# Optimization experiments

Measured on AMD Instinct MI355X. Metric: run time of the kernel, lower is better.

## Reference

```python
import jax, jax.numpy as jnp
import numpy as np

B, F, P = 16384, 4096, 32
D = F // P
EPS = 1e-5


def setup_inputs() -> dict:
    key = jax.random.key(0)
    ks = jax.random.split(key, 5)
    bound = 1.0 / np.sqrt(D)
    return {
        "x": jax.random.normal(ks[0], (B, F), dtype=jnp.float32),
        "weights1": jax.random.uniform(ks[1], (P, D, D), dtype=jnp.float32, minval=-bound, maxval=bound),
        "bias1": jax.random.uniform(ks[2], (F,), dtype=jnp.float32, minval=-bound, maxval=bound),
        "weights2": jax.random.uniform(ks[3], (P, D, D), dtype=jnp.float32, minval=-bound, maxval=bound),
        "bias2": jax.random.uniform(ks[4], (F,), dtype=jnp.float32, minval=-bound, maxval=bound),
        "gamma1": jnp.ones((F,), dtype=jnp.float32),
        "beta1": jnp.zeros((F,), dtype=jnp.float32),
        "gamma3": jnp.ones((F,), dtype=jnp.float32),
        "beta3": jnp.zeros((F,), dtype=jnp.float32),
    }


def _block_matmul(x, w):
    # x: [B, F] viewed as [B, P, D]; w: [P, D, D] block-diagonal blocks.
    # Equivalent to x @ block_diag(*w) without building the [F, F] matrix.
    xb = x.reshape(x.shape[0], P, D)
    return jnp.einsum("bpd,pde->bpe", xb, w).reshape(x.shape[0], F)


def _batchnorm(y, gamma, beta):
    # Training-mode BatchNorm1d: biased variance over the batch dim.
    mean = jnp.mean(y, axis=0)
    var = jnp.var(y, axis=0)
    return gamma * (y - mean) * jax.lax.rsqrt(var + EPS) + beta


def reference(x, weights1, bias1, weights2, bias2, gamma1, beta1, gamma3, beta3):
    o1 = jnp.tanh(_batchnorm(_block_matmul(x, weights1) + bias1, gamma1, beta1))
    o2 = _block_matmul(o1, weights2) + bias2
    o3 = jnp.tanh(_batchnorm(o2 + x, gamma3, beta3))
    return o3
```

## Files before the change

### kernel.cpp

```cpp
#include <hip/hip_runtime.h>
#include <hip/hip_bf16.h>
#include <cstdint>
#include <cstddef>

#define B_ 16384
#define F_ 4096
#define P_ 32
#define D_ 128
#define STRIPS 32
#define ITERS 8

using f32x4 = __attribute__((ext_vector_type(4))) float;
using s16x8 = __attribute__((ext_vector_type(8))) short;

union abuf { s16x8 v; uint32_t u[4]; };

__device__ inline uint32_t pk_bf16(float a, float b) {
    float2 f; f.x = a; f.y = b;
    union { __hip_bfloat162 h; uint32_t u; } cv;
    cv.h = __float22bfloat162_rn(f);
    return cv.u;
}
__device__ inline float tanh_e(float ze) {
    float e = __builtin_amdgcn_exp2f(ze);
    return 1.f - 2.f * __builtin_amdgcn_rcpf(e + 1.f);
}

__device__ inline void stage_wp(const float* __restrict__ Wp, short* s_w, int tid) {
#pragma unroll
    for (int it = 0; it < 8; ++it) {
        int slot = it * 256 + tid;
        int l15 = slot & 15;
        int l4  = (slot >> 4) & 3;
        int sp  = (slot >> 6) & 3;
        int j   = slot >> 8;
        const float* s0 = Wp + (size_t)(sp * 32 + l4 * 4) * D_ + j * 16 + l15;
        const float* s1 = s0 + (size_t)16 * D_;
        abuf a;
        a.u[0] = pk_bf16(s0[0],            s0[(size_t)D_]);
        a.u[1] = pk_bf16(s0[(size_t)2*D_], s0[(size_t)3*D_]);
        a.u[2] = pk_bf16(s1[0],            s1[(size_t)D_]);
        a.u[3] = pk_bf16(s1[(size_t)2*D_], s1[(size_t)3*D_]);
        *(s16x8*)((char*)s_w + (size_t)slot * 16) = a.v;
    }
}

__global__ __launch_bounds__(256, 3) void k_stats1(
    const float* __restrict__ x, const float* __restrict__ W1,
    float* __restrict__ gsum, float* __restrict__ gsq)
{
    __shared__ short s_w[D_ * D_];
    __shared__ float s_sum[D_], s_sq[D_];
    const int tid = threadIdx.x;
    const int p = blockIdx.x / STRIPS, strip = blockIdx.x % STRIPS;
    stage_wp(W1 + (size_t)p * D_ * D_, s_w, tid);
    if (tid < D_) { s_sum[tid] = 0.f; s_sq[tid] = 0.f; }
    __syncthreads();
    const int wave = tid >> 6, lane = tid & 63;
    const int l15 = lane & 15, l4 = lane >> 4;
    const int ldsb = lane * 16;

    f32x4 csum[8], csq[8];
#pragma unroll
    for (int j = 0; j < 8; ++j) { csum[j] = (f32x4){0,0,0,0}; csq[j] = (f32x4){0,0,0,0}; }

    for (int it = 0; it < ITERS; ++it) {
        const int g = strip * 32 + it * 4 + wave;
        const float* ap = x + (size_t)(g * 16 + l15) * F_ + p * D_ + l4 * 4;
        f32x4 xv[8];
#pragma unroll
        for (int j = 0; j < 8; ++j)
            xv[j] = __builtin_nontemporal_load((const f32x4*)(ap + j * 16));
        abuf a[4];
#pragma unroll
        for (int s = 0; s < 4; ++s) {
            a[s].u[0] = pk_bf16(xv[2*s][0],   xv[2*s][1]);
            a[s].u[1] = pk_bf16(xv[2*s][2],   xv[2*s][3]);
            a[s].u[2] = pk_bf16(xv[2*s+1][0], xv[2*s+1][1]);
            a[s].u[3] = pk_bf16(xv[2*s+1][2], xv[2*s+1][3]);
        }
        f32x4 acc[8];
#pragma unroll
        for (int j = 0; j < 8; ++j) acc[j] = (f32x4){0,0,0,0};
#pragma unroll
        for (int s = 0; s < 4; ++s)
#pragma unroll
            for (int j = 0; j < 8; ++j) {
                s16x8 w = *(const s16x8*)((const char*)s_w + (j * 4 + s) * 1024 + ldsb);
                acc[j] = __builtin_amdgcn_mfma_f32_16x16x32_bf16(w, a[s].v, acc[j], 0, 0, 0);
            }
#pragma unroll
        for (int j = 0; j < 8; ++j)
#pragma unroll
            for (int r = 0; r < 4; ++r) {
                float v = acc[j][r];
                csum[j][r] += v;
                csq[j][r] = fmaf(v, v, csq[j][r]);
            }
    }
#pragma unroll
    for (int j = 0; j < 8; ++j)
#pragma unroll
        for (int r = 0; r < 4; ++r) {
            float sm = csum[j][r], q = csq[j][r];
            sm += __shfl_xor(sm, 1); q += __shfl_xor(q, 1);
            sm += __shfl_xor(sm, 2); q += __shfl_xor(q, 2);
            sm += __shfl_xor(sm, 4); q += __shfl_xor(q, 4);
            sm += __shfl_xor(sm, 8); q += __shfl_xor(q, 8);
            if (l15 == 0) {
                atomicAdd(&s_sum[j * 16 + l4 * 4 + r], sm);
                atomicAdd(&s_sq [j * 16 + l4 * 4 + r], q);
            }
        }
    __syncthreads();
    if (tid < D_) {
        atomicAdd(&gsum[p * D_ + tid], s_sum[tid]);
        atomicAdd(&gsq [p * D_ + tid], s_sq[tid]);
    }
}

__global__ __launch_bounds__(256, 2) void k_fused(
    const float* __restrict__ x, float* __restrict__ yf,
    const float* __restrict__ W1, const float* __restrict__ W2,
    const float* __restrict__ sce, const float* __restrict__ she,
    float* __restrict__ gsum, float* __restrict__ gsq)
{
    __shared__ short s_w1[D_ * D_];
    __shared__ short s_w2[D_ * D_];
    __shared__ float s_sc[D_], s_sh[D_];
    __shared__ float s_sum[D_], s_sq[D_];
    const int tid = threadIdx.x;
    const int p = blockIdx.x / STRIPS, strip = blockIdx.x % STRIPS;
    stage_wp(W1 + (size_t)p * D_ * D_, s_w1, tid);
    stage_wp(W2 + (size_t)p * D_ * D_, s_w2, tid);
    if (tid < D_) {
        s_sc[tid] = sce[p * D_ + tid];
        s_sh[tid] = she[p * D_ + tid];
        s_sum[tid] = 0.f; s_sq[tid] = 0.f;
    }
    __syncthreads();
    const int wave = tid >> 6, lane = tid & 63;
    const int l15 = lane & 15, l4 = lane >> 4;
    const int ldsb = lane * 16;

    f32x4 csum[8], csq[8];
#pragma unroll
    for (int j = 0; j < 8; ++j) { csum[j] = (f32x4){0,0,0,0}; csq[j] = (f32x4){0,0,0,0}; }

    auto LOADX = [&](f32x4 (&xv)[8], int it) {
        const int g = strip * 32 + it * 4 + wave;
        const float* ap = x + (size_t)(g * 16 + l15) * F_ + p * D_ + l4 * 4;
#pragma unroll
        for (int j = 0; j < 8; ++j)
            xv[j] = __builtin_nontemporal_load((const f32x4*)(ap + j * 16));
    };

    auto TILE = [&](f32x4 (&xv)[8], int it) {
        abuf a[4];
#pragma unroll
        for (int s = 0; s < 4; ++s) {
            a[s].u[0] = pk_bf16(xv[2*s][0],   xv[2*s][1]);
            a[s].u[1] = pk_bf16(xv[2*s][2],   xv[2*s][3]);
            a[s].u[2] = pk_bf16(xv[2*s+1][0], xv[2*s+1][1]);
            a[s].u[3] = pk_bf16(xv[2*s+1][2], xv[2*s+1][3]);
        }
        f32x4 acc[8];
#pragma unroll
        for (int j = 0; j < 8; ++j) acc[j] = (f32x4){0,0,0,0};
#pragma unroll
        for (int s = 0; s < 4; ++s)
#pragma unroll
            for (int j = 0; j < 8; ++j) {
                s16x8 w = *(const s16x8*)((const char*)s_w1 + (j * 4 + s) * 1024 + ldsb);
                acc[j] = __builtin_amdgcn_mfma_f32_16x16x32_bf16(w, a[s].v, acc[j], 0, 0, 0);
            }
#pragma unroll
        for (int sp = 0; sp < 4; ++sp) {
            const int kb = sp * 32 + l4 * 4;
            f32x4 sc0 = *(const f32x4*)&s_sc[kb], sc1 = *(const f32x4*)&s_sc[kb + 16];
            f32x4 sh0 = *(const f32x4*)&s_sh[kb], sh1 = *(const f32x4*)&s_sh[kb + 16];
            float t0[4], t1[4];
#pragma unroll
            for (int q = 0; q < 4; ++q) {
                t0[q] = tanh_e(fmaf(acc[2*sp][q],   sc0[q], sh0[q]));
                t1[q] = tanh_e(fmaf(acc[2*sp+1][q], sc1[q], sh1[q]));
            }
            a[sp].u[0] = pk_bf16(t0[0], t0[1]);
            a[sp].u[1] = pk_bf16(t0[2], t0[3]);
            a[sp].u[2] = pk_bf16(t1[0], t1[1]);
            a[sp].u[3] = pk_bf16(t1[2], t1[3]);
        }
#pragma unroll
        for (int j = 0; j < 8; ++j) acc[j] = (f32x4){0,0,0,0};
#pragma unroll
        for (int sp = 0; sp < 4; ++sp)
#pragma unroll
            for (int j = 0; j < 8; ++j) {
                s16x8 w = *(const s16x8*)((const char*)s_w2 + (j * 4 + sp) * 1024 + ldsb);
                acc[j] = __builtin_amdgcn_mfma_f32_16x16x32_bf16(w, a[sp].v, acc[j], 0, 0, 0);
            }
        const int g = strip * 32 + it * 4 + wave;
        float* rp = yf + (size_t)(g * 16 + l15) * F_ + p * D_ + l4 * 4;
#pragma unroll
        for (int j = 0; j < 8; ++j) {
            f32x4 o;
#pragma unroll
            for (int r = 0; r < 4; ++r) {
                float v = acc[j][r] + xv[j][r];
                o[r] = v;
                csum[j][r] += v;
                csq[j][r] = fmaf(v, v, csq[j][r]);
            }
            __builtin_nontemporal_store(o, (f32x4*)(rp + j * 16));
        }
    };

    f32x4 xv0[8], xv1[8];
    LOADX(xv0, 0);
#pragma unroll
    for (int h = 0; h < 4; ++h) {
        LOADX(xv1, 2 * h + 1);
        TILE(xv0, 2 * h);
        if (h < 3) LOADX(xv0, 2 * h + 2);
        TILE(xv1, 2 * h + 1);
    }

#pragma unroll
    for (int j = 0; j < 8; ++j)
#pragma unroll
        for (int r = 0; r < 4; ++r) {
            float sm = csum[j][r], q = csq[j][r];
            sm += __shfl_xor(sm, 1); q += __shfl_xor(q, 1);
            sm += __shfl_xor(sm, 2); q += __shfl_xor(q, 2);
            sm += __shfl_xor(sm, 4); q += __shfl_xor(q, 4);
            sm += __shfl_xor(sm, 8); q += __shfl_xor(q, 8);
            if (l15 == 0) {
                atomicAdd(&s_sum[j * 16 + l4 * 4 + r], sm);
                atomicAdd(&s_sq [j * 16 + l4 * 4 + r], q);
            }
        }
    __syncthreads();
    if (tid < D_) {
        atomicAdd(&gsum[p * D_ + tid], s_sum[tid]);
        atomicAdd(&gsq [p * D_ + tid], s_sq[tid]);
    }
}

__global__ void k_finalize(const float* __restrict__ sum,
                           const float* __restrict__ sumsq,
                           const float* __restrict__ gamma,
                           const float* __restrict__ beta,
                           float* __restrict__ sce, float* __restrict__ she)
{
    const float L2E2 = 2.f * 1.44269504088896340736f;
    int f = blockIdx.x * blockDim.x + threadIdx.x;
    if (f < F_) {
        float mean = sum[f] * (1.f / B_);
        float var  = sumsq[f] * (1.f / B_) - mean * mean;
        float rstd = rsqrtf(var + 1e-5f);
        float sc = gamma[f] * rstd;
        sce[f] = L2E2 * sc;
        she[f] = L2E2 * (beta[f] - mean * sc);
    }
}

__global__ void k_bn_tanh(float* yb, const float* __restrict__ sce,
                          const float* __restrict__ she)
{
    const size_t n4 = (size_t)B_ * F_ / 4;
    size_t i = (size_t)blockIdx.x * blockDim.x + threadIdx.x;
    const size_t stride = (size_t)gridDim.x * blockDim.x;
    for (; i < n4; i += stride) {
        f32x4 v = __builtin_nontemporal_load((const f32x4*)yb + i);
        int col = (int)((i * 4) & (F_ - 1));
        f32x4 sc = *(const f32x4*)(sce + col);
        f32x4 sh = *(const f32x4*)(she + col);
        f32x4 r;
#pragma unroll
        for (int t = 0; t < 4; ++t) r[t] = tanh_e(fmaf(v[t], sc[t], sh[t]));
        __builtin_nontemporal_store(r, (f32x4*)yb + i);
    }
}

extern "C" void kernel_launch(void* const* d_in, const int* in_sizes, int n_in,
                              void* d_out, int out_size, void* d_ws, size_t ws_size,
                              hipStream_t stream) {
    const float* x      = (const float*)d_in[0];
    const float* W1     = (const float*)d_in[1];
    const float* W2     = (const float*)d_in[3];
    const float* gamma1 = (const float*)d_in[5];
    const float* beta1  = (const float*)d_in[6];
    const float* gamma3 = (const float*)d_in[7];
    const float* beta3  = (const float*)d_in[8];

    float* yf = (float*)d_out;
    float* S  = (float*)d_ws;
    float* sum1 = S;
    float* sq1  = S + 4096;
    float* sum3 = S + 8192;
    float* sq3  = S + 12288;
    float* sce1 = S + 16384;
    float* she1 = S + 20480;
    float* sce3 = S + 24576;
    float* she3 = S + 28672;

    hipMemsetAsync(d_ws, 0, 4 * 4096 * sizeof(float), stream);

    k_stats1<<<P_ * STRIPS, 256, 0, stream>>>(x, W1, sum1, sq1);
    k_finalize<<<F_ / 256, 256, 0, stream>>>(sum1, sq1, gamma1, beta1, sce1, she1);
    k_fused<<<P_ * STRIPS, 256, 0, stream>>>(x, yf, W1, W2, sce1, she1, sum3, sq3);
    k_finalize<<<F_ / 256, 256, 0, stream>>>(sum3, sq3, gamma3, beta3, sce3, she3);
    k_bn_tanh<<<4096, 256, 0, stream>>>(yf, sce3, she3);
}
```

Measured before the change: 627.2 us.

## Store pre-BN intermediate as fp16 in workspace and software-pipeline stats1 loads

The fused kernel now writes the pre-normalization residual sum as fp16 into workspace rather than fp32 into the output, and the final BN+tanh pass reads fp16 and writes fp32 output. This halves the intermediate's write and read traffic, at the cost of fp16 rounding before normalization. The first stats kernel also gets double-buffered x loads with occupancy hint lowered to 2, and nontemporal hints are dropped on x loads. The fp16 path runs only if the workspace is large enough.

```diff
diff --git a/kernel.cpp b/kernel.cpp
--- a/kernel.cpp
+++ b/kernel.cpp
@@ -1,5 +1,6 @@
 #include <hip/hip_runtime.h>
 #include <hip/hip_bf16.h>
+#include <hip/hip_fp16.h>
 #include <cstdint>
 #include <cstddef>
 
@@ -20,6 +21,16 @@
     union { __hip_bfloat162 h; uint32_t u; } cv;
     cv.h = __float22bfloat162_rn(f);
     return cv.u;
+}
+__device__ inline uint32_t pk_f16(float a, float b) {
+    float2 f; f.x = a; f.y = b;
+    union { __half2 h; uint32_t u; } cv;
+    cv.h = __float22half2_rn(f);
+    return cv.u;
+}
+__device__ inline float f16_f32(unsigned short h) {
+    union { unsigned short u; __half h; } cv; cv.u = h;
+    return __half2float(cv.h);
 }
 __device__ inline float tanh_e(float ze) {
     float e = __builtin_amdgcn_exp2f(ze);
@@ -45,7 +56,7 @@
     }
 }
 
-__global__ __launch_bounds__(256, 3) void k_stats1(
+__global__ __launch_bounds__(256, 2) void k_stats1(
     const float* __restrict__ x, const float* __restrict__ W1,
     float* __restrict__ gsum, float* __restrict__ gsq)
 {
@@ -64,13 +75,15 @@
 #pragma unroll
     for (int j = 0; j < 8; ++j) { csum[j] = (f32x4){0,0,0,0}; csq[j] = (f32x4){0,0,0,0}; }
 
-    for (int it = 0; it < ITERS; ++it) {
+    auto LOADX = [&](f32x4 (&xv)[8], int it) {
         const int g = strip * 32 + it * 4 + wave;
         const float* ap = x + (size_t)(g * 16 + l15) * F_ + p * D_ + l4 * 4;
-        f32x4 xv[8];
 #pragma unroll
         for (int j = 0; j < 8; ++j)
-            xv[j] = __builtin_nontemporal_load((const f32x4*)(ap + j * 16));
+            xv[j] = *(const f32x4*)(ap + j * 16);
+    };
+
+    auto TILE = [&](f32x4 (&xv)[8]) {
         abuf a[4];
 #pragma unroll
         for (int s = 0; s < 4; ++s) {
@@ -97,7 +110,18 @@
                 csum[j][r] += v;
                 csq[j][r] = fmaf(v, v, csq[j][r]);
             }
-    }
+    };
+
+    f32x4 xv0[8], xv1[8];
+    LOADX(xv0, 0);
+#pragma unroll
+    for (int h = 0; h < 4; ++h) {
+        LOADX(xv1, 2 * h + 1);
+        TILE(xv0);
+        if (h < 3) LOADX(xv0, 2 * h + 2);
+        TILE(xv1);
+    }
+
 #pragma unroll
     for (int j = 0; j < 8; ++j)
 #pragma unroll
@@ -119,8 +143,10 @@
     }
 }
 
+template<bool FH>
 __global__ __launch_bounds__(256, 2) void k_fused(
     const float* __restrict__ x, float* __restrict__ yf,
+    unsigned short* __restrict__ yh,
     const float* __restrict__ W1, const float* __restrict__ W2,
     const float* __restrict__ sce, const float* __restrict__ she,
     float* __restrict__ gsum, float* __restrict__ gsq)
@@ -152,7 +178,7 @@
         const float* ap = x + (size_t)(g * 16 + l15) * F_ + p * D_ + l4 * 4;
 #pragma unroll
         for (int j = 0; j < 8; ++j)
-            xv[j] = __builtin_nontemporal_load((const f32x4*)(ap + j * 16));
+            xv[j] = *(const f32x4*)(ap + j * 16);
     };
 
     auto TILE = [&](f32x4 (&xv)[8], int it) {
@@ -200,7 +226,7 @@
                 acc[j] = __builtin_amdgcn_mfma_f32_16x16x32_bf16(w, a[sp].v, acc[j], 0, 0, 0);
             }
         const int g = strip * 32 + it * 4 + wave;
-        float* rp = yf + (size_t)(g * 16 + l15) * F_ + p * D_ + l4 * 4;
+        const size_t rowoff = (size_t)(g * 16 + l15) * F_ + p * D_ + l4 * 4;
 #pragma unroll
         for (int j = 0; j < 8; ++j) {
             f32x4 o;
@@ -211,7 +237,15 @@
                 csum[j][r] += v;
                 csq[j][r] = fmaf(v, v, csq[j][r]);
             }
-            __builtin_nontemporal_store(o, (f32x4*)(rp + j * 16));
+            if (FH) {
+                uint32_t h2[2];
+                h2[0] = pk_f16(o[0], o[1]);
+                h2[1] = pk_f16(o[2], o[3]);
+                __builtin_nontemporal_store(*(const uint64_t*)h2,
+                                            (uint64_t*)(yh + rowoff + j * 16));
+            } else {
+                __builtin_nontemporal_store(o, (f32x4*)(yf + rowoff + j * 16));
+            }
         }
     };
 
@@ -264,21 +298,44 @@
     }
 }
 
-__global__ void k_bn_tanh(float* yb, const float* __restrict__ sce,
+template<bool FH>
+__global__ void k_bn_tanh(const unsigned short* __restrict__ yh,
+                          float* __restrict__ out,
+                          const float* __restrict__ sce,
                           const float* __restrict__ she)
 {
-    const size_t n4 = (size_t)B_ * F_ / 4;
-    size_t i = (size_t)blockIdx.x * blockDim.x + threadIdx.x;
-    const size_t stride = (size_t)gridDim.x * blockDim.x;
-    for (; i < n4; i += stride) {
-        f32x4 v = __builtin_nontemporal_load((const f32x4*)yb + i);
-        int col = (int)((i * 4) & (F_ - 1));
-        f32x4 sc = *(const f32x4*)(sce + col);
-        f32x4 sh = *(const f32x4*)(she + col);
-        f32x4 r;
-#pragma unroll
-        for (int t = 0; t < 4; ++t) r[t] = tanh_e(fmaf(v[t], sc[t], sh[t]));
-        __builtin_nontemporal_store(r, (f32x4*)yb + i);
+    if (FH) {
+        const size_t n8 = (size_t)B_ * F_ / 8;
+        size_t i = (size_t)blockIdx.x * blockDim.x + threadIdx.x;
+        const size_t stride = (size_t)gridDim.x * blockDim.x;
+        for (; i < n8; i += stride) {
+            s16x8 hv = *(const s16x8*)(yh + i * 8);
+            int col = (int)((i * 8) & (F_ - 1));
+            f32x4 sc0 = *(const f32x4*)(sce + col), sc1 = *(const f32x4*)(sce + col + 4);
+            f32x4 sh0 = *(const f32x4*)(she + col), sh1 = *(const f32x4*)(she + col + 4);
+            f32x4 r0, r1;
+#pragma unroll
+            for (int t = 0; t < 4; ++t) {
+                r0[t] = tanh_e(fmaf(f16_f32((unsigned short)hv[t]),     sc0[t], sh0[t]));
+                r1[t] = tanh_e(fmaf(f16_f32((unsigned short)hv[t + 4]), sc1[t], sh1[t]));
+            }
+            __builtin_nontemporal_store(r0, (f32x4*)(out + i * 8));
+            __builtin_nontemporal_store(r1, (f32x4*)(out + i * 8 + 4));
+        }
+    } else {
+        const size_t n4 = (size_t)B_ * F_ / 4;
+        size_t i = (size_t)blockIdx.x * blockDim.x + threadIdx.x;
+        const size_t stride = (size_t)gridDim.x * blockDim.x;
+        for (; i < n4; i += stride) {
+            f32x4 v = ((const f32x4*)out)[i];
+            int col = (int)((i * 4) & (F_ - 1));
+            f32x4 sc = *(const f32x4*)(sce + col);
+            f32x4 sh = *(const f32x4*)(she + col);
+            f32x4 r;
+#pragma unroll
+            for (int t = 0; t < 4; ++t) r[t] = tanh_e(fmaf(v[t], sc[t], sh[t]));
+            __builtin_nontemporal_store(r, (f32x4*)out + i);
+        }
     }
 }
 
@@ -303,12 +360,21 @@
     float* she1 = S + 20480;
     float* sce3 = S + 24576;
     float* she3 = S + 28672;
+    unsigned short* yh = (unsigned short*)((char*)d_ws + 128 * 1024);
+
+    const bool fh = ws_size >= (size_t)128 * 1024 + (size_t)B_ * F_ * 2;
 
     hipMemsetAsync(d_ws, 0, 4 * 4096 * sizeof(float), stream);
 
     k_stats1<<<P_ * STRIPS, 256, 0, stream>>>(x, W1, sum1, sq1);
     k_finalize<<<F_ / 256, 256, 0, stream>>>(sum1, sq1, gamma1, beta1, sce1, she1);
-    k_fused<<<P_ * STRIPS, 256, 0, stream>>>(x, yf, W1, W2, sce1, she1, sum3, sq3);
-    k_finalize<<<F_ / 256, 256, 0, stream>>>(sum3, sq3, gamma3, beta3, sce3, she3);
-    k_bn_tanh<<<4096, 256, 0, stream>>>(yf, sce3, she3);
-}
+    if (fh) {
+        k_fused<true><<<P_ * STRIPS, 256, 0, stream>>>(x, yf, yh, W1, W2, sce1, she1, sum3, sq3);
+        k_finalize<<<F_ / 256, 256, 0, stream>>>(sum3, sq3, gamma3, beta3, sce3, she3);
+        k_bn_tanh<true><<<4096, 256, 0, stream>>>(yh, yf, sce3, she3);
+    } else {
+        k_fused<false><<<P_ * STRIPS, 256, 0, stream>>>(x, yf, yh, W1, W2, sce1, she1, sum3, sq3);
+        k_finalize<<<F_ / 256, 256, 0, stream>>>(sum3, sq3, gamma3, beta3, sce3, she3);
+        k_bn_tanh<false><<<4096, 256, 0, stream>>>((const unsigned short*)yf, yf, sce3, she3);
+    }
+}
```

Result: faster. 559.8 us (-10.7%).
